# Kernel tuning notes

Measured on AMD Instinct MI355X. Metric: run time of the kernel, lower is better.

## Reference

```python
import jax, jax.numpy as jnp
import numpy as np

B = 2
DIMS = ((41, 800, 800), (21, 400, 400), (11, 200, 200), (6, 100, 100))  # (D,H,W)=(z,y,x) per level
VS = ((0.1, 0.1, 0.2), (0.2, 0.2, 0.4), (0.4, 0.4, 0.8), (0.8, 0.8, 1.6))  # (vx,vy,vz)
OFFSET = (0.0, -40.0, -3.0)  # world offset (x,y,z)
BN_EPS = 1e-3

OFFS27 = jnp.array([[z, y, x] for z in (-1, 0, 1) for y in (-1, 0, 1) for x in (-1, 0, 1)], jnp.int32)

# ---------------- numpy-side input construction ----------------

def _np_downsample(coords, out_dims):
    # active output sites of SparseConv3d(k=3, s=2, p=1): in = 2*o - 1 + kd, kd in 0..2
    outs = []
    for kz in range(3):
        for ky in range(3):
            for kx in range(3):
                o = coords[:, 1:] + 1 - np.array([kz, ky, kx])
                ok = (o % 2 == 0).all(1)
                oc = o // 2
                ok &= (oc >= 0).all(1)
                ok &= (oc[:, 0] < out_dims[0]) & (oc[:, 1] < out_dims[1]) & (oc[:, 2] < out_dims[2])
                outs.append(np.concatenate([coords[ok, :1], oc[ok]], 1))
    return np.unique(np.concatenate(outs, 0), axis=0).astype(np.int32)


def _make_coords(rng):
    per_batch = []
    D0, H0, W0 = DIMS[0]
    for b in range(B):
        nc = 120
        centers = np.stack([rng.integers(3, D0 - 4, nc), rng.integers(5, H0 - 6, nc), rng.integers(5, W0 - 6, nc)], 1)
        offs = rng.integers(-3, 4, (nc, 40, 3))
        p = np.clip((centers[:, None, :] + offs).reshape(-1, 3), 0, np.array(DIMS[0]) - 1)
        p = np.unique(p, axis=0)  # sorted lexicographically == sorted by linear key
        per_batch.append(np.concatenate([np.full((len(p), 1), b), p], 1))
    return np.concatenate(per_batch, 0).astype(np.int32)


def setup_inputs():
    rng = np.random.default_rng(0)
    coords0 = _make_coords(rng)
    coords1 = _np_downsample(coords0, DIMS[1])
    coords2 = _np_downsample(coords1, DIMS[2])
    coords3 = _np_downsample(coords2, DIMS[3])
    n = coords0.shape[0]
    c = coords0.astype(np.float64)
    x = OFFSET[0] + (c[:, 3] + 0.5) * VS[0][0] + rng.uniform(-0.04, 0.04, n)
    y = OFFSET[1] + (c[:, 2] + 0.5) * VS[0][1] + rng.uniform(-0.04, 0.04, n)
    z = OFFSET[2] + (c[:, 1] + 0.5) * VS[0][2] + rng.uniform(-0.08, 0.08, n)
    vf = np.stack([x, y, z, rng.uniform(0.0, 1.0, n)], 1).astype(np.float32)

    def conv_w(k, cin, cout):
        return (rng.standard_normal((k, cin, cout)) / np.sqrt(k * cin)).astype(np.float32)

    def bn_p(ch):
        return np.stack([1.0 + 0.05 * rng.standard_normal(ch), 0.05 * rng.standard_normal(ch)], 0).astype(np.float32)

    inp = dict(voxel_features=vf, coords0=coords0, coords1=coords1, coords2=coords2, coords3=coords3,
               w00=conv_w(27, 4, 16), b00=bn_p(16), w01=conv_w(27, 16, 16), b01=bn_p(16),
               wd0=conv_w(27, 16, 32), bd0=bn_p(32),
               w10=conv_w(27, 32, 32), b10=bn_p(32), w11=conv_w(27, 32, 32), b11=bn_p(32),
               wd1=conv_w(27, 32, 64), bd1=bn_p(64),
               w20=conv_w(27, 64, 64), b20=bn_p(64), w21=conv_w(27, 64, 64), b21=bn_p(64), w22=conv_w(27, 64, 64), b22=bn_p(64),
               wd2=conv_w(27, 64, 64), bd2=bn_p(64),
               w30=conv_w(27, 64, 64), b30=bn_p(64), w31=conv_w(27, 64, 64), b31=bn_p(64), w32=conv_w(27, 64, 64), b32=bn_p(64),
               we=(rng.standard_normal((64, 64)) / 8.0).astype(np.float32), be=bn_p(64),
               fc_w=(rng.standard_normal((64, 160)) / np.sqrt(160.0)).astype(np.float32),
               cls_w=(rng.standard_normal((1, 64)) / 8.0).astype(np.float32),
               reg_w=(rng.standard_normal((3, 64)) / 8.0).astype(np.float32))
    return {k: jnp.asarray(v) for k, v in inp.items()}

# ---------------- jax sparse-conv primitives ----------------

def _key(c, dims):
    D, H, W = dims
    return ((c[:, 0] * D + c[:, 1]) * H + c[:, 2]) * W + c[:, 3]


def _gather(nb_b, nb, feats, keys_sorted, dims):
    # nb: (N,27,3) candidate (z,y,x); gather rows of feats via sorted-key lookup, zeros if absent
    D, H, W = dims
    inb = (nb[..., 0] >= 0) & (nb[..., 0] < D) & (nb[..., 1] >= 0) & (nb[..., 1] < H) & (nb[..., 2] >= 0) & (nb[..., 2] < W)
    nbc = jnp.clip(nb, 0, jnp.array(dims, jnp.int32) - 1)
    qk = ((nb_b * D + nbc[..., 0]) * H + nbc[..., 1]) * W + nbc[..., 2]
    pos = jnp.clip(jnp.searchsorted(keys_sorted, qk), 0, keys_sorted.shape[0] - 1)
    found = inb & (keys_sorted[pos] == qk)
    return jnp.where(found[..., None], feats[pos], 0.0)


def _subm(feats, coords, keys, dims, w):
    nb = coords[:, None, 1:] + OFFS27[None]
    g = _gather(coords[:, None, 0], nb, feats, keys, dims)  # (N,27,Cin)
    return jnp.einsum('nkc,kco->no', g, w)


def _stride(feats, in_keys, in_dims, coords_out, w):
    nb = coords_out[:, None, 1:] * 2 + OFFS27[None]  # in = 2*o - 1 + kd
    g = _gather(coords_out[:, None, 0], nb, feats, in_keys, in_dims)
    return jnp.einsum('nkc,kco->no', g, w)


def _bn_relu(x, p):
    # train-mode BatchNorm1d over active voxels (biased var), eps=1e-3
    m = x.mean(0)
    v = jnp.mean((x - m) ** 2, 0)
    return jax.nn.relu((x - m) * jax.lax.rsqrt(v + BN_EPS) * p[0] + p[1])


def _t2p(coords, vs):
    c = coords.astype(jnp.float32)
    x = OFFSET[0] + (c[:, 3] + 0.5) * vs[0]
    y = OFFSET[1] + (c[:, 2] + 0.5) * vs[1]
    z = OFFSET[2] + (c[:, 1] + 0.5) * vs[2]
    return jnp.stack([c[:, 0], x, y, z], 1)


def _nn_interp(unknown, known, feats):
    # three_nn (squared L2, batch-separated, non-differentiable) + three_interpolate
    d2 = jnp.sum((unknown[:, None, 1:] - known[None, :, 1:]) ** 2, -1)
    d2 = d2 + 1e10 * (unknown[:, None, 0] != known[None, :, 0])
    d2 = jax.lax.stop_gradient(d2)
    negd, idx = jax.lax.top_k(-d2, 3)
    w = 1.0 / (-negd + 1e-8)
    w = w / w.sum(1, keepdims=True)
    return jnp.sum(feats[idx] * w[..., None], 1)


def _forward(voxel_features, w00, b00, w01, b01, wd0, bd0, w10, b10, w11, b11, wd1, bd1,
             w20, b20, w21, b21, w22, b22, wd2, bd2, w30, b30, w31, b31, w32, b32,
             we, be, fc_w, cls_w, reg_w, coords0, coords1, coords2, coords3):
    k0, k1 = _key(coords0, DIMS[0]), _key(coords1, DIMS[1])
    k2 = _key(coords2, DIMS[2])
    points_mean = jnp.concatenate([coords0[:, :1].astype(jnp.float32), voxel_features[:, :3]], 1)
    f = _bn_relu(_subm(voxel_features, coords0, k0, DIMS[0], w00), b00)
    f = _bn_relu(_subm(f, coords0, k0, DIMS[0], w01), b01)
    f = _bn_relu(_stride(f, k0, DIMS[0], coords1, wd0), bd0)
    f = _bn_relu(_subm(f, coords1, k1, DIMS[1], w10), b10)
    f = _bn_relu(_subm(f, coords1, k1, DIMS[1], w11), b11)
    p1 = _nn_interp(points_mean, _t2p(coords1, VS[1]), f)
    f = _bn_relu(_stride(f, k1, DIMS[1], coords2, wd1), bd1)
    f = _bn_relu(_subm(f, coords2, k2, DIMS[2], w20), b20)
    f = _bn_relu(_subm(f, coords2, k2, DIMS[2], w21), b21)
    f = _bn_relu(_subm(f, coords2, k2, DIMS[2], w22), b22)
    p2 = _nn_interp(points_mean, _t2p(coords2, VS[2]), f)
    f = _bn_relu(_stride(f, k2, DIMS[2], coords3, wd2), bd2)
    k3 = _key(coords3, DIMS[3])
    f = _bn_relu(_subm(f, coords3, k3, DIMS[3], w30), b30)
    f = _bn_relu(_subm(f, coords3, k3, DIMS[3], w31), b31)
    f = _bn_relu(_subm(f, coords3, k3, DIMS[3], w32), b32)
    p3 = _nn_interp(points_mean, _t2p(coords3, VS[3]), f)
    out = _bn_relu(f @ we, be)  # extra_conv: 1x1x1 SparseConv3d
    D3, H3, W3 = DIMS[3]
    dense = jnp.zeros((B, D3, H3, W3, 64), out.dtype).at[coords3[:, 0], coords3[:, 1], coords3[:, 2], coords3[:, 3]].set(out)
    xd = dense.transpose(0, 4, 1, 2, 3).reshape(B, 64 * D3, H3, W3)  # (N, C*D, H, W)
    pw = jnp.concatenate([p1, p2, p3], 1) @ fc_w.T
    return (xd, points_mean, pw @ cls_w.T, pw @ reg_w.T)


def reference(voxel_features, w00, b00, w01, b01, wd0, bd0, w10, b10, w11, b11, wd1, bd1,
              w20, b20, w21, b21, w22, b22, wd2, bd2, w30, b30, w31, b31, w32, b32,
              we, be, fc_w, cls_w, reg_w, coords0, coords1, coords2, coords3):
    return _forward(voxel_features, w00, b00, w01, b01, wd0, bd0, w10, b10, w11, b11, wd1, bd1,
                    w20, b20, w21, b21, w22, b22, wd2, bd2, w30, b30, w31, b31, w32, b32,
                    we, be, fc_w, cls_w, reg_w, coords0, coords1, coords2, coords3)
```

## Files before the change

kernel.cpp:

```cpp
#include <hip/hip_runtime.h>

#define OFFX 0.0f
#define OFFY -40.0f
#define OFFZ -3.0f
#define BNEPS 1e-3f
#define NCH 128
#define NG 9

typedef _Float16 h2_t __attribute__((ext_vector_type(2)));
__device__ inline h2_t u2h(unsigned u) { union { unsigned u; h2_t h; } x; x.u = u; return x.h; }
__device__ inline unsigned h2u(h2_t h) { union { unsigned u; h2_t h; } x; x.h = h; return x.u; }

struct PrepA {
  const int *c0, *c1, *c2, *c3;
  int n0, n1, n2, n3;
  int *k0, *k1, *k2, *k3;
  float4 *kp1, *kp2, *kp3;
  int* bs;
  const float* vf; float* pmb; float* out1;
  int* ctrs;
};
__global__ void prep_k(PrepA a) {
  int i = blockIdx.x * 256 + threadIdx.x;
  if (i < 16) a.ctrs[i] = 0;
  if (i < a.n0) {
    const int* c = a.c0 + (size_t)i * 4;
    a.k0[i] = ((c[0] * 41 + c[1]) * 800 + c[2]) * 800 + c[3];
    float b = (float)c[0];
    float x = a.vf[(size_t)i * 4], y = a.vf[(size_t)i * 4 + 1], z = a.vf[(size_t)i * 4 + 2];
    a.pmb[(size_t)i * 4] = b; a.pmb[(size_t)i * 4 + 1] = x;
    a.pmb[(size_t)i * 4 + 2] = y; a.pmb[(size_t)i * 4 + 3] = z;
    a.out1[(size_t)i * 4] = b; a.out1[(size_t)i * 4 + 1] = x;
    a.out1[(size_t)i * 4 + 2] = y; a.out1[(size_t)i * 4 + 3] = z;
  }
  if (i < a.n1) {
    const int* c = a.c1 + (size_t)i * 4;
    a.k1[i] = ((c[0] * 21 + c[1]) * 400 + c[2]) * 400 + c[3];
    a.kp1[i] = make_float4(OFFX + (c[3] + 0.5f) * 0.2f, OFFY + (c[2] + 0.5f) * 0.2f,
                           OFFZ + (c[1] + 0.5f) * 0.4f, (float)c[0]);
    if (c[0] == 0 && (i + 1 == a.n1 || a.c1[(size_t)(i + 1) * 4] == 1)) a.bs[0] = i + 1;
  }
  if (i < a.n2) {
    const int* c = a.c2 + (size_t)i * 4;
    a.k2[i] = ((c[0] * 11 + c[1]) * 200 + c[2]) * 200 + c[3];
    a.kp2[i] = make_float4(OFFX + (c[3] + 0.5f) * 0.4f, OFFY + (c[2] + 0.5f) * 0.4f,
                           OFFZ + (c[1] + 0.5f) * 0.8f, (float)c[0]);
    if (c[0] == 0 && (i + 1 == a.n2 || a.c2[(size_t)(i + 1) * 4] == 1)) a.bs[1] = i + 1;
  }
  if (i < a.n3) {
    const int* c = a.c3 + (size_t)i * 4;
    a.k3[i] = ((c[0] * 6 + c[1]) * 100 + c[2]) * 100 + c[3];
    a.kp3[i] = make_float4(OFFX + (c[3] + 0.5f) * 0.8f, OFFY + (c[2] + 0.5f) * 0.8f,
                           OFFZ + (c[1] + 0.5f) * 1.6f, (float)c[0]);
    if (c[0] == 0 && (i + 1 == a.n3 || a.c3[(size_t)(i + 1) * 4] == 1)) a.bs[2] = i + 1;
  }
}

struct NbrE { const int* coords; int np; const int* keys; int nk; int D, H, W, scale; int* nbr; };
struct NbrA { NbrE e[7]; };
__global__ void nbra_k(NbrA a) {
  NbrE v = a.e[blockIdx.y];
  int t = blockIdx.x * 256 + threadIdx.x;
  if (t >= v.np * 9) return;
  int p = t / 9, j = t % 9;
  int kz = j / 3 - 1, ky = j % 3 - 1;
  const int* c = v.coords + (size_t)p * 4;
  int z = c[1] * v.scale + kz, y = c[2] * v.scale + ky;
  int xb = c[3] * v.scale - 1;
  int r[3] = {-1, -1, -1};
  if (z >= 0 && z < v.D && y >= 0 && y < v.H) {
    int qb = ((c[0] * v.D + z) * v.H + y) * v.W + xb;
    int lo = 0, hi = v.nk;
    const int* keys = v.keys;
    while (lo < hi) { int m = (lo + hi) >> 1; if (keys[m] < qb) lo = m + 1; else hi = m; }
#pragma unroll
    for (int dx = 0; dx < 3; dx++) {
      int q = qb + dx;
      int xq = xb + dx;
      if (lo < v.nk && keys[lo] == q) {
        if (xq >= 0 && xq < v.W) r[dx] = lo;
        lo++;
      }
    }
  }
  int* dst = v.nbr + (size_t)p * 27 + j * 3;
  dst[0] = r[0]; dst[1] = r[1]; dst[2] = r[2];
}

struct WPrep { const float* src; unsigned* dst; int cin; int cout; };
struct WP13 { WPrep l[13]; };
__global__ void wprep_k(WP13 a) {
  WPrep w = a.l[blockIdx.y];
  int cp2 = w.cin / 2;
  int tot = 27 * cp2 * w.cout;
  int i = blockIdx.x * 256 + threadIdx.x;
  if (i >= tot) return;
  int o = i % w.cout, rest = i / w.cout;
  int cp = rest % cp2, k = rest / cp2;
  float lo = w.src[((size_t)k * w.cin + 2 * cp) * w.cout + o];
  float hi = w.src[((size_t)k * w.cin + 2 * cp + 1) * w.cout + o];
  h2_t h; h[0] = (_Float16)lo; h[1] = (_Float16)hi;
  w.dst[i] = h2u(h);
}

template<int CIN, int COUT>
__global__ __launch_bounds__(128) void convg_k(const float* __restrict__ feats,
                                               const int* __restrict__ nbr,
                                               const float* __restrict__ w, int n,
                                               float* __restrict__ partial, int gstride) {
  constexpr int TP = 32;
  constexpr int LDP = 36;
  constexpr int CO = COUT / 16;
  __shared__ float G[CIN * LDP];
  int tid = threadIdx.x;
  int pg = tid >> 4, cg = tid & 15;
  int p0 = blockIdx.x * TP;
  int k0 = blockIdx.y * 3;
  float acc[4][CO];
#pragma unroll
  for (int i = 0; i < 4; i++)
#pragma unroll
    for (int j = 0; j < CO; j++) acc[i][j] = 0.f;

  for (int kk = 0; kk < 3; kk++) {
    int k = k0 + kk;
    __syncthreads();
    for (int ch = tid; ch < TP * CIN / 4; ch += 128) {
      int r = ch & (TP - 1), c4 = ch / TP;
      int p = p0 + r;
      int idx = (p < n) ? nbr[(size_t)p * 27 + k] : -1;
      float4 fv = make_float4(0.f, 0.f, 0.f, 0.f);
      if (idx >= 0) fv = *(const float4*)(feats + (size_t)idx * CIN + c4 * 4);
      G[(c4 * 4 + 0) * LDP + r] = fv.x;
      G[(c4 * 4 + 1) * LDP + r] = fv.y;
      G[(c4 * 4 + 2) * LDP + r] = fv.z;
      G[(c4 * 4 + 3) * LDP + r] = fv.w;
    }
    __syncthreads();
    const float* wk = w + (size_t)k * CIN * COUT + cg * CO;
#pragma unroll
    for (int c = 0; c < CIN; c++) {
      float4 g4 = *(const float4*)&G[c * LDP + pg * 4];
      float wv[CO];
      if constexpr (CO == 4)      *(float4*)wv = *(const float4*)(wk + c * COUT);
      else if constexpr (CO == 2) *(float2*)wv = *(const float2*)(wk + c * COUT);
      else                        wv[0] = wk[c * COUT];
      float gp[4] = {g4.x, g4.y, g4.z, g4.w};
#pragma unroll
      for (int i = 0; i < 4; i++)
#pragma unroll
        for (int j = 0; j < CO; j++) acc[i][j] = fmaf(gp[i], wv[j], acc[i][j]);
    }
  }
#pragma unroll
  for (int i = 0; i < 4; i++) {
    int p = p0 + pg * 4 + i;
    if (p < n) {
      float* dst = partial + (size_t)blockIdx.y * gstride + (size_t)p * COUT + cg * CO;
      if constexpr (CO == 4)      *(float4*)dst = *(float4*)acc[i];
      else if constexpr (CO == 2) *(float2*)dst = *(float2*)acc[i];
      else                        dst[0] = acc[i][0];
    }
  }
}

template<int CIN, int COUT>
__global__ __launch_bounds__(128) void convh_k(const unsigned* __restrict__ fh,
                                               const int* __restrict__ nbr,
                                               const unsigned* __restrict__ wh, int n,
                                               void* __restrict__ partial, int gstride,
                                               const float* __restrict__ scsh) {
  constexpr int TP = 32;
  constexpr int LDPH = 36;
  constexpr int CO = COUT / 16;
  constexpr int CP = CIN / 2;
  constexpr bool H2P = (CO >= 2);
  __shared__ unsigned H[CP * LDPH];
  int tid = threadIdx.x;
  int pg = tid >> 4, cg = tid & 15;
  int p0 = blockIdx.x * TP;
  int k0 = blockIdx.y * 3;
  int r = tid & 31;
  int p = p0 + r;
  int sidx[3];
  if (p < n) {
    const int* nb = nbr + (size_t)p * 27 + k0;
    sidx[0] = nb[0]; sidx[1] = nb[1]; sidx[2] = nb[2];
  } else { sidx[0] = sidx[1] = sidx[2] = -1; }

  float acc[4][CO];
#pragma unroll
  for (int i = 0; i < 4; i++)
#pragma unroll
    for (int j = 0; j < CO; j++) acc[i][j] = 0.f;

  if constexpr (CIN >= 32) {
    constexpr int NLD = CIN / 32;
    uint4 pf[NLD];
    {
      int idx = sidx[0];
#pragma unroll
      for (int it = 0; it < NLD; it++) {
        int q = (tid >> 5) + it * 4;
        pf[it] = (idx >= 0) ? *(const uint4*)(fh + (size_t)idx * CP + q * 4)
                            : make_uint4(0, 0, 0, 0);
      }
    }
    for (int kk = 0; kk < 3; kk++) {
      bool ok = sidx[kk] >= 0;
      __syncthreads();
#pragma unroll
      for (int it = 0; it < NLD; it++) {
        int q = (tid >> 5) + it * 4;
        unsigned uu[4] = {pf[it].x, pf[it].y, pf[it].z, pf[it].w};
#pragma unroll
        for (int j = 0; j < 4; j++) {
          int cp = q * 4 + j;
          unsigned outw = 0;
          if (ok) {
            h2_t h = u2h(uu[j]);
            float lo = fmaxf(fmaf((float)h[0], scsh[2 * cp], scsh[CIN + 2 * cp]), 0.f);
            float hi = fmaxf(fmaf((float)h[1], scsh[2 * cp + 1], scsh[CIN + 2 * cp + 1]), 0.f);
            h2_t o; o[0] = (_Float16)lo; o[1] = (_Float16)hi;
            outw = h2u(o);
          }
          H[cp * LDPH + r] = outw;
        }
      }
      if (kk < 2) {
        int idx = sidx[kk + 1];
#pragma unroll
        for (int it = 0; it < NLD; it++) {
          int q = (tid >> 5) + it * 4;
          pf[it] = (idx >= 0) ? *(const uint4*)(fh + (size_t)idx * CP + q * 4)
                              : make_uint4(0, 0, 0, 0);
        }
      }
      __syncthreads();
      const unsigned* wk = wh + (size_t)(k0 + kk) * CP * COUT + cg * CO;
#pragma unroll 8
      for (int cp = 0; cp < CP; cp++) {
        uint4 g4 = *(const uint4*)&H[cp * LDPH + pg * 4];
        unsigned gg[4] = {g4.x, g4.y, g4.z, g4.w};
        unsigned wv[CO];
        if constexpr (CO == 4)      *(uint4*)wv = *(const uint4*)(wk + cp * COUT);
        else if constexpr (CO == 2) *(uint2*)wv = *(const uint2*)(wk + cp * COUT);
        else                        wv[0] = wk[cp * COUT];
#pragma unroll
        for (int i = 0; i < 4; i++)
#pragma unroll
          for (int j = 0; j < CO; j++)
            acc[i][j] = __builtin_amdgcn_fdot2(u2h(gg[i]), u2h(wv[j]), acc[i][j], false);
      }
    }
  } else {
    int q = tid >> 5;
    uint2 pf2;
    {
      int idx = sidx[0];
      pf2 = (idx >= 0) ? *(const uint2*)(fh + (size_t)idx * CP + q * 2) : make_uint2(0, 0);
    }
    for (int kk = 0; kk < 3; kk++) {
      bool ok = sidx[kk] >= 0;
      __syncthreads();
      unsigned uu[2] = {pf2.x, pf2.y};
#pragma unroll
      for (int j = 0; j < 2; j++) {
        int cp = q * 2 + j;
        unsigned outw = 0;
        if (ok) {
          h2_t h = u2h(uu[j]);
          float lo = fmaxf(fmaf((float)h[0], scsh[2 * cp], scsh[CIN + 2 * cp]), 0.f);
          float hi = fmaxf(fmaf((float)h[1], scsh[2 * cp + 1], scsh[CIN + 2 * cp + 1]), 0.f);
          h2_t o; o[0] = (_Float16)lo; o[1] = (_Float16)hi;
          outw = h2u(o);
        }
        H[cp * LDPH + r] = outw;
      }
      if (kk < 2) {
        int idx = sidx[kk + 1];
        pf2 = (idx >= 0) ? *(const uint2*)(fh + (size_t)idx * CP + q * 2) : make_uint2(0, 0);
      }
      __syncthreads();
      const unsigned* wk = wh + (size_t)(k0 + kk) * CP * COUT + cg * CO;
#pragma unroll
      for (int cp = 0; cp < CP; cp++) {
        uint4 g4 = *(const uint4*)&H[cp * LDPH + pg * 4];
        unsigned gg[4] = {g4.x, g4.y, g4.z, g4.w};
        unsigned wv[CO];
        if constexpr (CO == 4)      *(uint4*)wv = *(const uint4*)(wk + cp * COUT);
        else if constexpr (CO == 2) *(uint2*)wv = *(const uint2*)(wk + cp * COUT);
        else                        wv[0] = wk[cp * COUT];
#pragma unroll
        for (int i = 0; i < 4; i++)
#pragma unroll
          for (int j = 0; j < CO; j++)
            acc[i][j] = __builtin_amdgcn_fdot2(u2h(gg[i]), u2h(wv[j]), acc[i][j], false);
      }
    }
  }
#pragma unroll
  for (int i = 0; i < 4; i++) {
    int pp = p0 + pg * 4 + i;
    if (pp < n) {
      if constexpr (H2P) {
        unsigned* dst = (unsigned*)partial + (size_t)blockIdx.y * gstride
                      + (size_t)pp * (COUT / 2) + cg * (CO / 2);
        if constexpr (CO == 4) {
          h2_t a; a[0] = (_Float16)acc[i][0]; a[1] = (_Float16)acc[i][1];
          h2_t b; b[0] = (_Float16)acc[i][2]; b[1] = (_Float16)acc[i][3];
          *(uint2*)dst = make_uint2(h2u(a), h2u(b));
        } else {
          h2_t a; a[0] = (_Float16)acc[i][0]; a[1] = (_Float16)acc[i][1];
          dst[0] = h2u(a);
        }
      } else {
        float* dst = (float*)partial + (size_t)blockIdx.y * gstride
                   + (size_t)pp * COUT + cg * CO;
        dst[0] = acc[i][0];
      }
    }
  }
}

template<bool H2P>
__global__ void bn_k(const void* __restrict__ partial, int G, int gstride, int n, int C,
                     float* __restrict__ pre, unsigned* __restrict__ preh,
                     float* __restrict__ stats, const float* __restrict__ bnp,
                     float* __restrict__ scsh, int* __restrict__ ctr) {
  __shared__ float l1e[256], l2e[256], l1o[256], l2o[256];
  __shared__ int lastf;
  int t = threadIdx.x;
  int total = n * C;
  float s1e = 0.f, s2e = 0.f, s1o = 0.f, s2o = 0.f;
  for (int i2 = (blockIdx.x * 256 + t) * 2; i2 < total; i2 += NCH * 512) {
    float v0 = 0.f, v1 = 0.f;
    if constexpr (H2P) {
      const unsigned* ph = (const unsigned*)partial;
      for (int g = 0; g < G; g++) {
        h2_t h = u2h(ph[(size_t)g * gstride + (i2 >> 1)]);
        v0 += (float)h[0]; v1 += (float)h[1];
      }
    } else {
      const float* pf = (const float*)partial;
      for (int g = 0; g < G; g++) {
        float2 pv = *(const float2*)(pf + (size_t)g * gstride + i2);
        v0 += pv.x; v1 += pv.y;
      }
    }
    if (pre) *(float2*)(pre + i2) = make_float2(v0, v1);
    h2_t h; h[0] = (_Float16)v0; h[1] = (_Float16)v1;
    preh[i2 >> 1] = h2u(h);
    s1e += v0; s2e += v0 * v0; s1o += v1; s2o += v1 * v1;
  }
  l1e[t] = s1e; l2e[t] = s2e; l1o[t] = s1o; l2o[t] = s2o;
  for (int s = 128; s >= C / 2; s >>= 1) {
    __syncthreads();
    if (t < s) {
      l1e[t] += l1e[t + s]; l2e[t] += l2e[t + s];
      l1o[t] += l1o[t + s]; l2o[t] += l2o[t + s];
    }
  }
  __syncthreads();
  if (t < C / 2) {
    stats[((size_t)blockIdx.x * C + 2 * t) * 2]     = l1e[t];
    stats[((size_t)blockIdx.x * C + 2 * t) * 2 + 1] = l2e[t];
    stats[((size_t)blockIdx.x * C + 2 * t + 1) * 2]     = l1o[t];
    stats[((size_t)blockIdx.x * C + 2 * t + 1) * 2 + 1] = l2o[t];
  }
  __threadfence();
  __syncthreads();
  if (t == 0) lastf = (atomicAdd(ctr, 1) == NCH - 1) ? 1 : 0;
  __syncthreads();
  if (lastf) {
    __threadfence();
    int c = t % C, sub = t / C;
    int TPC = 256 / C;
    float a1 = 0.f, a2 = 0.f;
    for (int ch = sub; ch < NCH; ch += TPC) {
      a1 += stats[((size_t)ch * C + c) * 2];
      a2 += stats[((size_t)ch * C + c) * 2 + 1];
    }
    l1e[t] = a1; l2e[t] = a2;
    for (int s = 128; s >= C; s >>= 1) {
      __syncthreads();
      if (t < s) { l1e[t] += l1e[t + s]; l2e[t] += l2e[t + s]; }
    }
    __syncthreads();
    if (t < C) {
      float m = l1e[t] / n;
      float v = l2e[t] / n - m * m;
      float sc = bnp[t] / sqrtf(v + BNEPS);
      scsh[t] = sc;
      scsh[C + t] = bnp[C + t] - m * sc;
    }
  }
}

__global__ __launch_bounds__(256) void knni_k(const float4* __restrict__ pm4, int n0,
                                              const float4* __restrict__ kp4, int nl,
                                              const int* __restrict__ bsp,
                                              const unsigned* __restrict__ fh, int C,
                                              const float* __restrict__ scsh,
                                              float* __restrict__ X, int xoff) {
  __shared__ __align__(16) float4 kp[512];
  __shared__ int bl[4], bh[4];
  int tid = threadIdx.x;
  int wave = tid >> 6, lane = tid & 63;
  int u = blockIdx.x * 4 + wave;
  bool valid = u < n0;
  float4 up = pm4[valid ? u : (n0 - 1)];
  int bs = bsp[0];
  int lo = (up.x == 0.f) ? 0 : bs;
  int hi = (up.x == 0.f) ? bs : nl;
  if (!valid) { lo = 0; hi = 0; }
  if (lane == 0) { bl[wave] = valid ? lo : 0x7fffffff; bh[wave] = valid ? hi : 0; }
  __syncthreads();
  int blo = min(min(bl[0], bl[1]), min(bl[2], bl[3]));
  int bhi = max(max(bh[0], bh[1]), max(bh[2], bh[3]));
  float ux = up.y, uy = up.z, uz = up.w;
  float d0 = 3e38f, d1 = 3e38f, d2 = 3e38f;
  int i0 = -1, i1 = -1, i2 = -1;
#define INS1(DD, GI) { \
    bool l0 = (DD) < d0, l1 = (DD) < d1, l2 = (DD) < d2; \
    i2 = l2 ? (l1 ? i1 : (GI)) : i2; \
    i1 = l1 ? (l0 ? i0 : (GI)) : i1; \
    i0 = l0 ? (GI) : i0; \
    float t1_ = __builtin_amdgcn_fmed3f(d0, d1, (DD)); \
    float t2_ = __builtin_amdgcn_fmed3f(d1, d2, (DD)); \
    d0 = fminf(d0, (DD)); d1 = t1_; d2 = t2_; }
#define DIST(Q) fmaf(ux - (Q).x, ux - (Q).x, fmaf(uy - (Q).y, uy - (Q).y, (uz - (Q).z) * (uz - (Q).z)))
  for (int cb = blo; cb < bhi; cb += 512) {
    int m = bhi - cb; if (m > 512) m = 512;
    __syncthreads();
    for (int i = tid; i < m; i += 256) kp[i] = kp4[cb + i];
    __syncthreads();
    if (cb + 512 <= lo || cb >= hi) continue;
    if (m == 512 && cb >= lo && cb + 512 <= hi) {
#pragma unroll
      for (int b = 0; b < 512; b += 256) {
        float4 q0 = kp[b + lane], q1 = kp[b + lane + 64];
        float4 q2 = kp[b + lane + 128], q3 = kp[b + lane + 192];
        float a0 = DIST(q0), a1 = DIST(q1), a2 = DIST(q2), a3 = DIST(q3);
        if (__any((a0 < d2) | (a1 < d2) | (a2 < d2) | (a3 < d2))) {
          INS1(a0, cb + b + lane) INS1(a1, cb + b + lane + 64)
          INS1(a2, cb + b + lane + 128) INS1(a3, cb + b + lane + 192)
        }
      }
    } else {
#pragma unroll
      for (int j = 0; j < 8; j++) {
        int i = lane + 64 * j;
        int e = cb + i;
        if (i < m && e >= lo && e < hi) {
          float4 q = kp[i];
          float dd = DIST(q);
          INS1(dd, e)
        }
      }
    }
  }
#pragma unroll
  for (int off = 1; off < 64; off <<= 1) {
    float e0 = __shfl_xor(d0, off), e1 = __shfl_xor(d1, off), e2 = __shfl_xor(d2, off);
    int j0 = __shfl_xor(i0, off), j1 = __shfl_xor(i1, off), j2 = __shfl_xor(i2, off);
    INS1(e0, j0) INS1(e1, j1) INS1(e2, j2)
  }
#undef DIST
#undef INS1
  i0 = __shfl(i0, 0); i1 = __shfl(i1, 0); i2 = __shfl(i2, 0);
  d0 = __shfl(d0, 0); d1 = __shfl(d1, 0); d2 = __shfl(d2, 0);
  if (valid && i0 >= 0) {
    float w0 = 1.f / (d0 + 1e-8f), w1 = 1.f / (d1 + 1e-8f), w2 = 1.f / (d2 + 1e-8f);
    float s = w0 + w1 + w2;
    w0 /= s; w1 /= s; w2 /= s;
    int CP = C >> 1;
    for (int cp = lane; cp < CP; cp += 64) {
      h2_t h0 = u2h(fh[(size_t)i0 * CP + cp]);
      h2_t h1 = u2h(fh[(size_t)i1 * CP + cp]);
      h2_t h2v = u2h(fh[(size_t)i2 * CP + cp]);
      int ce = 2 * cp, co = 2 * cp + 1;
      float se = scsh[ce], he = scsh[C + ce];
      float so = scsh[co], ho = scsh[C + co];
      float ae = w0 * fmaxf(fmaf((float)h0[0], se, he), 0.f)
               + w1 * fmaxf(fmaf((float)h1[0], se, he), 0.f)
               + w2 * fmaxf(fmaf((float)h2v[0], se, he), 0.f);
      float ao = w0 * fmaxf(fmaf((float)h0[1], so, ho), 0.f)
               + w1 * fmaxf(fmaf((float)h1[1], so, ho), 0.f)
               + w2 * fmaxf(fmaf((float)h2v[1], so, ho), 0.f);
      *(float2*)(X + (size_t)u * 160 + xoff + ce) = make_float2(ae, ao);
    }
  }
}

__global__ __launch_bounds__(256) void conv1x1_k(const unsigned* __restrict__ fh,
                                                 const float* __restrict__ scsh,
                                                 const float* __restrict__ we, int n,
                                                 float* __restrict__ out) {
  __shared__ float rows[256];
  int t = threadIdx.x;
  int p = blockIdx.x * 4 + (t >> 6), c = t & 63;
  float v = 0.f;
  if (p < n) {
    h2_t h = u2h(fh[(size_t)p * 32 + (c >> 1)]);
    v = fmaxf(fmaf((float)h[c & 1], scsh[c], scsh[64 + c]), 0.f);
  }
  rows[t] = v;
  __syncthreads();
  if (p >= n) return;
  const float* fr = rows + (t >> 6) * 64;
  float a = 0.f;
#pragma unroll 16
  for (int ci = 0; ci < 64; ci++) a = fmaf(fr[ci], we[ci * 64 + c], a);
  out[(size_t)p * 64 + c] = a;
}

__global__ void scatter_k(const float* __restrict__ pre, const float* __restrict__ scsh,
                          const int* __restrict__ c3, int n3, float* __restrict__ out0) {
  int t = blockIdx.x * 256 + threadIdx.x;
  if (t >= n3 * 64) return;
  int p = t >> 6, c = t & 63;
  const int* cc = c3 + (size_t)p * 4;
  size_t o = ((((size_t)cc[0] * 64 + c) * 6 + cc[1]) * 100 + cc[2]) * 100 + cc[3];
  out0[o] = fmaxf(fmaf(pre[t], scsh[c], scsh[64 + c]), 0.f);
}

__global__ __launch_bounds__(256) void head_k(const float* __restrict__ X,
                                              const float* __restrict__ fcw,
                                              const float* __restrict__ clsw,
                                              const float* __restrict__ regw,
                                              int n0, float* __restrict__ outc,
                                              float* __restrict__ outr) {
  __shared__ float fl[64 * 161];
  int t = threadIdx.x;
  for (int i = t; i < 64 * 160; i += 256) {
    int r = i / 160, c = i % 160;
    fl[r * 161 + c] = fcw[i];
  }
  __syncthreads();
  int wave = t >> 6, lane = t & 63;
  int u = blockIdx.x * 4 + wave;
  if (u >= n0) return;
  const float* xr = X + (size_t)u * 160;
  const float* wr = fl + (size_t)lane * 161;
  float a = 0.f;
#pragma unroll 8
  for (int i = 0; i < 160; i++) a = fmaf(xr[i], wr[i], a);
  float c = a * clsw[lane];
  float r0 = a * regw[lane], r1 = a * regw[64 + lane], r2 = a * regw[128 + lane];
  for (int off = 32; off; off >>= 1) {
    c  += __shfl_down(c, off);
    r0 += __shfl_down(r0, off);
    r1 += __shfl_down(r1, off);
    r2 += __shfl_down(r2, off);
  }
  if (lane == 0) {
    outc[u] = c;
    outr[(size_t)u * 3] = r0; outr[(size_t)u * 3 + 1] = r1; outr[(size_t)u * 3 + 2] = r2;
  }
}

extern "C" void kernel_launch(void* const* d_in, const int* in_sizes, int n_in,
                              void* d_out, int out_size, void* d_ws, size_t ws_size,
                              hipStream_t stream) {
  const float* vf  = (const float*)d_in[0];
  const int* c0 = (const int*)d_in[1];
  const int* c1 = (const int*)d_in[2];
  const int* c2 = (const int*)d_in[3];
  const int* c3 = (const int*)d_in[4];
  const float* w00 = (const float*)d_in[5];  const float* b00 = (const float*)d_in[6];
  const float* w01 = (const float*)d_in[7];  const float* b01 = (const float*)d_in[8];
  const float* wd0 = (const float*)d_in[9];  const float* bd0 = (const float*)d_in[10];
  const float* w10 = (const float*)d_in[11]; const float* b10 = (const float*)d_in[12];
  const float* w11 = (const float*)d_in[13]; const float* b11 = (const float*)d_in[14];
  const float* wd1 = (const float*)d_in[15]; const float* bd1 = (const float*)d_in[16];
  const float* w20 = (const float*)d_in[17]; const float* b20 = (const float*)d_in[18];
  const float* w21 = (const float*)d_in[19]; const float* b21 = (const float*)d_in[20];
  const float* w22 = (const float*)d_in[21]; const float* b22 = (const float*)d_in[22];
  const float* wd2 = (const float*)d_in[23]; const float* bd2 = (const float*)d_in[24];
  const float* w30 = (const float*)d_in[25]; const float* b30 = (const float*)d_in[26];
  const float* w31 = (const float*)d_in[27]; const float* b31 = (const float*)d_in[28];
  const float* w32 = (const float*)d_in[29]; const float* b32 = (const float*)d_in[30];
  const float* we  = (const float*)d_in[31]; const float* be  = (const float*)d_in[32];
  const float* fcw = (const float*)d_in[33];
  const float* clsw = (const float*)d_in[34];
  const float* regw = (const float*)d_in[35];

  int N0 = in_sizes[1] / 4, N1 = in_sizes[2] / 4, N2 = in_sizes[3] / 4, N3 = in_sizes[4] / 4;
  int maxN = N0; if (N1 > maxN) maxN = N1; if (N2 > maxN) maxN = N2; if (N3 > maxN) maxN = N3;

  auto cdiv = [](int a, int b) { return (a + b - 1) / b; };
  char* p = (char*)d_ws;
  auto alloc = [&](size_t bytes) { char* r = p; p += (bytes + 255) & ~(size_t)255; return r; };

  int* keys0 = (int*)alloc((size_t)N0 * 4);
  int* keys1 = (int*)alloc((size_t)N1 * 4);
  int* keys2 = (int*)alloc((size_t)N2 * 4);
  int* keys3 = (int*)alloc((size_t)N3 * 4);
  int* nbr0  = (int*)alloc((size_t)N0 * 27 * 4);
  int* nbrs1 = (int*)alloc((size_t)N1 * 27 * 4);
  int* nbr1  = (int*)alloc((size_t)N1 * 27 * 4);
  int* nbrs2 = (int*)alloc((size_t)N2 * 27 * 4);
  int* nbr2  = (int*)alloc((size_t)N2 * 27 * 4);
  int* nbrs3 = (int*)alloc((size_t)N3 * 27 * 4);
  int* nbr3  = (int*)alloc((size_t)N3 * 27 * 4);
  float* FB = (float*)alloc((size_t)maxN * 64 * 4);
  float* FC = (float*)alloc((size_t)maxN * 64 * 4);
  unsigned* FAh = (unsigned*)alloc((size_t)maxN * 32 * 4);
  unsigned* FBh = (unsigned*)alloc((size_t)maxN * 32 * 4);
  float* stats = (float*)alloc((size_t)NCH * 64 * 2 * 4);
  float* SC = (float*)alloc((size_t)15 * 128 * 4);
  int* ctrs = (int*)alloc(16 * 4);
  float* X  = (float*)alloc((size_t)N0 * 160 * 4);
  float* pmb = (float*)alloc((size_t)N0 * 4 * 4);
  float4* kp1 = (float4*)alloc((size_t)N1 * 16);
  float4* kp2 = (float4*)alloc((size_t)N2 * 16);
  float4* kp3 = (float4*)alloc((size_t)N3 * 16);
  int* bsA = (int*)alloc(32);
  unsigned* whbuf = (unsigned*)alloc((size_t)452736 * 4);

  float* out0 = (float*)d_out;
  float* out1 = out0 + 7680000;
  float* outc = out1 + (size_t)N0 * 4;
  float* outr = outc + N0;
  void* partial = out0;

  auto scsh = [&](int L) { return SC + (size_t)L * 128; };

  const float* wsrc[13] = {w01, wd0, w10, w11, wd1, w20, w21, w22, wd2, w30, w31, w32, nullptr};
  int wcin[13]  = {16, 16, 32, 32, 32, 64, 64, 64, 64, 64, 64, 64, 0};
  int wcout[13] = {16, 32, 32, 32, 64, 64, 64, 64, 64, 64, 64, 64, 0};
  unsigned* wdst[13];
  size_t woff = 0;
  WP13 wp{};
  int nw = 12;
  for (int i = 0; i < nw; i++) {
    wdst[i] = whbuf + woff;
    wp.l[i] = WPrep{wsrc[i], wdst[i], wcin[i], wcout[i]};
    woff += (size_t)27 * (wcin[i] / 2) * wcout[i];
  }
  for (int i = nw; i < 13; i++) wp.l[i] = WPrep{w01, wdst[0], 16, 16};

  wprep_k<<<dim3(216, nw), 256, 0, stream>>>(wp);
  PrepA pa;
  pa.c0 = c0; pa.c1 = c1; pa.c2 = c2; pa.c3 = c3;
  pa.n0 = N0; pa.n1 = N1; pa.n2 = N2; pa.n3 = N3;
  pa.k0 = keys0; pa.k1 = keys1; pa.k2 = keys2; pa.k3 = keys3;
  pa.kp1 = kp1; pa.kp2 = kp2; pa.kp3 = kp3;
  pa.bs = bsA; pa.vf = vf; pa.pmb = pmb; pa.out1 = out1;
  pa.ctrs = ctrs;
  prep_k<<<cdiv(maxN, 256), 256, 0, stream>>>(pa);
  NbrA na;
  na.e[0] = NbrE{c0, N0, keys0, N0, 41, 800, 800, 1, nbr0};
  na.e[1] = NbrE{c1, N1, keys0, N0, 41, 800, 800, 2, nbrs1};
  na.e[2] = NbrE{c1, N1, keys1, N1, 21, 400, 400, 1, nbr1};
  na.e[3] = NbrE{c2, N2, keys1, N1, 21, 400, 400, 2, nbrs2};
  na.e[4] = NbrE{c2, N2, keys2, N2, 11, 200, 200, 1, nbr2};
  na.e[5] = NbrE{c3, N3, keys2, N2, 11, 200, 200, 2, nbrs3};
  na.e[6] = NbrE{c3, N3, keys3, N3, 6, 100, 100, 1, nbr3};
  nbra_k<<<dim3(cdiv(maxN * 9, 256), 7), 256, 0, stream>>>(na);

  auto convh = [&](const unsigned* fhin, const int* nb, int wi, int n, int cin, int cout,
                   const float* ss) {
    dim3 g(cdiv(n, 32), NG);
    int gs = (cout >= 32) ? n * cout / 2 : n * cout;
    const unsigned* wh = wdst[wi];
    if (cin == 16 && cout == 16)
      convh_k<16, 16><<<g, 128, 0, stream>>>(fhin, nb, wh, n, partial, gs, ss);
    else if (cin == 16 && cout == 32)
      convh_k<16, 32><<<g, 128, 0, stream>>>(fhin, nb, wh, n, partial, gs, ss);
    else if (cin == 32 && cout == 32)
      convh_k<32, 32><<<g, 128, 0, stream>>>(fhin, nb, wh, n, partial, gs, ss);
    else if (cin == 32 && cout == 64)
      convh_k<32, 64><<<g, 128, 0, stream>>>(fhin, nb, wh, n, partial, gs, ss);
    else
      convh_k<64, 64><<<g, 128, 0, stream>>>(fhin, nb, wh, n, partial, gs, ss);
  };
  auto bnp = [&](const float* bnpar, int n, int C, float* pre, unsigned* preh, int L, bool h2p) {
    int gs = h2p ? n * C / 2 : n * C;
    if (h2p)
      bn_k<true><<<NCH, 256, 0, stream>>>(partial, NG, gs, n, C, pre, preh, stats, bnpar,
                                          scsh(L), ctrs + L);
    else
      bn_k<false><<<NCH, 256, 0, stream>>>(partial, NG, gs, n, C, pre, preh, stats, bnpar,
                                           scsh(L), ctrs + L);
  };
  auto knn = [&](const float4* kp4, const int* bsl, int nl, const unsigned* fh, int C, int L,
                 int xoff) {
    knni_k<<<cdiv(N0, 4), 256, 0, stream>>>((const float4*)pmb, N0, kp4, nl, bsl,
                                            fh, C, scsh(L), X, xoff);
  };

  convg_k<4, 16><<<dim3(cdiv(N0, 32), NG), 128, 0, stream>>>(vf, nbr0, w00, N0,
                                                             (float*)partial, N0 * 16);
  bnp(b00, N0, 16, nullptr, FAh, 0, false);
  convh(FAh, nbr0, 0, N0, 16, 16, scsh(0));   bnp(b01, N0, 16, nullptr, FBh, 1, false);
  convh(FBh, nbrs1, 1, N1, 16, 32, scsh(1));  bnp(bd0, N1, 32, nullptr, FAh, 2, true);
  convh(FAh, nbr1, 2, N1, 32, 32, scsh(2));   bnp(b10, N1, 32, nullptr, FBh, 3, true);
  convh(FBh, nbr1, 3, N1, 32, 32, scsh(3));   bnp(b11, N1, 32, nullptr, FAh, 4, true);
  knn(kp1, bsA + 0, N1, FAh, 32, 4, 0);
  convh(FAh, nbrs2, 4, N2, 32, 64, scsh(4));  bnp(bd1, N2, 64, nullptr, FBh, 5, true);
  convh(FBh, nbr2, 5, N2, 64, 64, scsh(5));   bnp(b20, N2, 64, nullptr, FAh, 6, true);
  convh(FAh, nbr2, 6, N2, 64, 64, scsh(6));   bnp(b21, N2, 64, nullptr, FBh, 7, true);
  convh(FBh, nbr2, 7, N2, 64, 64, scsh(7));   bnp(b22, N2, 64, nullptr, FAh, 8, true);
  knn(kp2, bsA + 1, N2, FAh, 64, 8, 32);
  convh(FAh, nbrs3, 8, N3, 64, 64, scsh(8));  bnp(bd2, N3, 64, nullptr, FBh, 9, true);
  convh(FBh, nbr3, 9, N3, 64, 64, scsh(9));   bnp(b30, N3, 64, nullptr, FAh, 10, true);
  convh(FAh, nbr3, 10, N3, 64, 64, scsh(10)); bnp(b31, N3, 64, nullptr, FBh, 11, true);
  convh(FBh, nbr3, 11, N3, 64, 64, scsh(11)); bnp(b32, N3, 64, nullptr, FAh, 12, true);
  knn(kp3, bsA + 2, N3, FAh, 64, 12, 96);

  conv1x1_k<<<cdiv(N3, 4), 256, 0, stream>>>(FAh, scsh(12), we, N3, FC);
  bn_k<false><<<NCH, 256, 0, stream>>>(FC, 1, 0, N3, 64, FB, FBh, stats, be, scsh(13),
                                       ctrs + 13);
  hipMemsetAsync(d_out, 0, (size_t)7680000 * 4, stream);
  scatter_k<<<cdiv(N3 * 64, 256), 256, 0, stream>>>(FB, scsh(13), c3, N3, out0);
  head_k<<<cdiv(N0, 4), 256, 0, stream>>>(X, fcw, clsw, regw, N0, outc, outr);
}
```

Measured before the change: 817.6 us.

## Skip kernel offsets with no active neighbours in tile, drop gather prefetch

The sparse-conv gather/GEMM kernel now uses a block-wide __syncthreads_or to skip a kernel offset entirely when no point in the 32-point tile has a neighbour there. This avoids the gather, BN/ReLU staging and dot-product loop for empty offsets, which are common on sparse data. In exchange, the register prefetch of the next offset's features is removed, so gather latency is no longer overlapped with compute. The NCH constant also doubles, which changes some chunking elsewhere.

```diff
diff --git a/kernel.cpp b/kernel.cpp
--- a/kernel.cpp
+++ b/kernel.cpp
@@ -4,7 +4,7 @@
 #define OFFY -40.0f
 #define OFFZ -3.0f
 #define BNEPS 1e-3f
-#define NCH 128
+#define NCH 256
 #define NG 9
 
 typedef _Float16 h2_t __attribute__((ext_vector_type(2)));
@@ -194,25 +194,17 @@
 #pragma unroll
     for (int j = 0; j < CO; j++) acc[i][j] = 0.f;
 
-  if constexpr (CIN >= 32) {
-    constexpr int NLD = CIN / 32;
-    uint4 pf[NLD];
-    {
-      int idx = sidx[0];
+  for (int kk = 0; kk < 3; kk++) {
+    int idx = sidx[kk];
+    bool ok = idx >= 0;
+    if (!__syncthreads_or(ok ? 1 : 0)) continue;
+    if constexpr (CIN >= 32) {
+      constexpr int NLD = CIN / 32;
 #pragma unroll
       for (int it = 0; it < NLD; it++) {
         int q = (tid >> 5) + it * 4;
-        pf[it] = (idx >= 0) ? *(const uint4*)(fh + (size_t)idx * CP + q * 4)
-                            : make_uint4(0, 0, 0, 0);
-      }
-    }
-    for (int kk = 0; kk < 3; kk++) {
-      bool ok = sidx[kk] >= 0;
-      __syncthreads();
-#pragma unroll
-      for (int it = 0; it < NLD; it++) {
-        int q = (tid >> 5) + it * 4;
-        unsigned uu[4] = {pf[it].x, pf[it].y, pf[it].z, pf[it].w};
+        uint4 u = ok ? *(const uint4*)(fh + (size_t)idx * CP + q * 4) : make_uint4(0, 0, 0, 0);
+        unsigned uu[4] = {u.x, u.y, u.z, u.w};
 #pragma unroll
         for (int j = 0; j < 4; j++) {
           int cp = q * 4 + j;
@@ -227,43 +219,10 @@
           H[cp * LDPH + r] = outw;
         }
       }
-      if (kk < 2) {
-        int idx = sidx[kk + 1];
-#pragma unroll
-        for (int it = 0; it < NLD; it++) {
-          int q = (tid >> 5) + it * 4;
-          pf[it] = (idx >= 0) ? *(const uint4*)(fh + (size_t)idx * CP + q * 4)
-                              : make_uint4(0, 0, 0, 0);
-        }
-      }
-      __syncthreads();
-      const unsigned* wk = wh + (size_t)(k0 + kk) * CP * COUT + cg * CO;
-#pragma unroll 8
-      for (int cp = 0; cp < CP; cp++) {
-        uint4 g4 = *(const uint4*)&H[cp * LDPH + pg * 4];
-        unsigned gg[4] = {g4.x, g4.y, g4.z, g4.w};
-        unsigned wv[CO];
-        if constexpr (CO == 4)      *(uint4*)wv = *(const uint4*)(wk + cp * COUT);
-        else if constexpr (CO == 2) *(uint2*)wv = *(const uint2*)(wk + cp * COUT);
-        else                        wv[0] = wk[cp * COUT];
-#pragma unroll
-        for (int i = 0; i < 4; i++)
-#pragma unroll
-          for (int j = 0; j < CO; j++)
-            acc[i][j] = __builtin_amdgcn_fdot2(u2h(gg[i]), u2h(wv[j]), acc[i][j], false);
-      }
-    }
-  } else {
-    int q = tid >> 5;
-    uint2 pf2;
-    {
-      int idx = sidx[0];
-      pf2 = (idx >= 0) ? *(const uint2*)(fh + (size_t)idx * CP + q * 2) : make_uint2(0, 0);
-    }
-    for (int kk = 0; kk < 3; kk++) {
-      bool ok = sidx[kk] >= 0;
-      __syncthreads();
-      unsigned uu[2] = {pf2.x, pf2.y};
+    } else {
+      int q = tid >> 5;
+      uint2 u = ok ? *(const uint2*)(fh + (size_t)idx * CP + q * 2) : make_uint2(0, 0);
+      unsigned uu[2] = {u.x, u.y};
 #pragma unroll
       for (int j = 0; j < 2; j++) {
         int cp = q * 2 + j;
@@ -277,26 +236,22 @@
         }
         H[cp * LDPH + r] = outw;
       }
-      if (kk < 2) {
-        int idx = sidx[kk + 1];
-        pf2 = (idx >= 0) ? *(const uint2*)(fh + (size_t)idx * CP + q * 2) : make_uint2(0, 0);
-      }
-      __syncthreads();
-      const unsigned* wk = wh + (size_t)(k0 + kk) * CP * COUT + cg * CO;
-#pragma unroll
-      for (int cp = 0; cp < CP; cp++) {
-        uint4 g4 = *(const uint4*)&H[cp * LDPH + pg * 4];
-        unsigned gg[4] = {g4.x, g4.y, g4.z, g4.w};
-        unsigned wv[CO];
-        if constexpr (CO == 4)      *(uint4*)wv = *(const uint4*)(wk + cp * COUT);
-        else if constexpr (CO == 2) *(uint2*)wv = *(const uint2*)(wk + cp * COUT);
-        else                        wv[0] = wk[cp * COUT];
-#pragma unroll
-        for (int i = 0; i < 4; i++)
-#pragma unroll
-          for (int j = 0; j < CO; j++)
-            acc[i][j] = __builtin_amdgcn_fdot2(u2h(gg[i]), u2h(wv[j]), acc[i][j], false);
-      }
+    }
+    __syncthreads();
+    const unsigned* wk = wh + (size_t)(k0 + kk) * CP * COUT + cg * CO;
+#pragma unroll 8
+    for (int cp = 0; cp < CP; cp++) {
+      uint4 g4 = *(const uint4*)&H[cp * LDPH + pg * 4];
+      unsigned gg[4] = {g4.x, g4.y, g4.z, g4.w};
+      unsigned wv[CO];
+      if constexpr (CO == 4)      *(uint4*)wv = *(const uint4*)(wk + cp * COUT);
+      else if constexpr (CO == 2) *(uint2*)wv = *(const uint2*)(wk + cp * COUT);
+      else                        wv[0] = wk[cp * COUT];
+#pragma unroll
+      for (int i = 0; i < 4; i++)
+#pragma unroll
+        for (int j = 0; j < CO; j++)
+          acc[i][j] = __builtin_amdgcn_fdot2(u2h(gg[i]), u2h(wv[j]), acc[i][j], false);
     }
   }
 #pragma unroll
```

Result: slower. 982.3 us (+20.1%).
